# Optimization experiments

Measured on AMD Instinct MI355X. Metric: run time of the kernel, lower is better.

Reference implementation:

```python
import jax, jax.numpy as jnp
import numpy as np

BIG = 1e9  # masks out invalid points in the NN search


def _pixel_grid(H, W, dtype):
    xs, ys = jnp.meshgrid(jnp.arange(W, dtype=dtype), jnp.arange(H, dtype=dtype), indexing='xy')
    return jnp.stack([xs.ravel(), ys.ravel(), jnp.ones(H * W, dtype)], axis=0)  # [3, N]


def _project(depth, K, pose_src, pose_dst, pix):
    """depth [B,1,H,W] -> (points in src cam frame [B,3,N], same points in dst cam frame [B,3,N])."""
    B = depth.shape[0]
    N = pix.shape[1]
    d = depth.reshape(B, 1, N)
    cam = jnp.einsum('bij,jn->bin', jnp.linalg.inv(K), pix) * d          # back-project
    homog = jnp.concatenate([cam, jnp.ones((B, 1, N), cam.dtype)], axis=1)
    T = jnp.einsum('bij,bjk->bik', jnp.linalg.inv(pose_dst), pose_src)   # dst <- src
    dst = jnp.einsum('bij,bjn->bin', T, homog)
    return cam, dst[:, :3]


def _masked_chamfer(a, b, ma, mb):
    """a [N,3], b [M,3], ma [N], mb [M] (0/1 floats). Squared-distance bidirectional chamfer,
    mean over valid points in each direction (pytorch3d chamfer_distance semantics on the
    masked subsets)."""
    d2 = jnp.sum(a * a, -1)[:, None] + jnp.sum(b * b, -1)[None, :] - 2.0 * (a @ b.T)  # [N,M]
    d_ab = jnp.min(d2 + (1.0 - mb)[None, :] * BIG, axis=1)  # NN in b for each a
    d_ba = jnp.min(d2 + (1.0 - ma)[:, None] * BIG, axis=0)  # NN in a for each b
    na = jnp.maximum(jnp.sum(ma), 1.0)
    nb = jnp.maximum(jnp.sum(mb), 1.0)
    return jnp.sum(d_ab * ma) / na + jnp.sum(d_ba * mb) / nb


def setup_inputs() -> dict:
    B, V, H, W = 2, 3, 64, 64
    key = jax.random.key(0)
    k1, k2, k3 = jax.random.split(key, 3)
    views = jax.random.normal(k1, (B, V, 3, H, W), jnp.float32)
    depth_maps = jax.random.uniform(k2, (B, V, 1, H, W), jnp.float32, 1.0, 4.0)
    masks = (jax.random.uniform(k3, (B, V, 1, H, W)) < 0.5).astype(jnp.float32)
    # pinhole intrinsics
    K = np.array([[64.0, 0.0, 32.0], [0.0, 64.0, 32.0], [0.0, 0.0, 1.0]], np.float32)
    intrinsics = jnp.asarray(np.tile(K, (B, 1, 1)))
    # valid SE(3) poses via Rodrigues
    rng = np.random.default_rng(0)
    poses = np.tile(np.eye(4, dtype=np.float32), (B, V, 1, 1))
    for b in range(B):
        for v in range(V):
            ax = rng.normal(size=3); ax = ax / np.linalg.norm(ax)
            ang = rng.uniform(-0.3, 0.3)
            Kx = np.array([[0, -ax[2], ax[1]], [ax[2], 0, -ax[0]], [-ax[1], ax[0], 0]])
            R = np.eye(3) + np.sin(ang) * Kx + (1 - np.cos(ang)) * (Kx @ Kx)
            poses[b, v, :3, :3] = R.astype(np.float32)
            poses[b, v, :3, 3] = rng.uniform(-0.5, 0.5, 3).astype(np.float32)
    return {"views": views, "poses": jnp.asarray(poses), "masks": masks,
            "intrinsics": intrinsics, "depth_maps": depth_maps, "num_views": 3}


def reference(views, poses, masks, intrinsics, depth_maps, num_views):
    B, V, _, H, W = depth_maps.shape
    pix = _pixel_grid(H, W, depth_maps.dtype)
    ref_pose = poses[:, 0]
    ref_mask = masks[:, 0].reshape(B, -1)
    ref_depth = depth_maps[:, 0]
    chamfer = jax.vmap(_masked_chamfer)
    geometric_loss = 0.0
    for i in range(1, num_views):
        tgt_mask = masks[:, i].reshape(B, -1)
        target_coord, proj_t2r = _project(depth_maps[:, i], intrinsics, poses[:, i], ref_pose, pix)
        ref_coord, proj_r2t = _project(ref_depth, intrinsics, ref_pose, poses[:, i], pix)
        fwd = chamfer(ref_coord.transpose(0, 2, 1), proj_t2r.transpose(0, 2, 1), ref_mask, tgt_mask)
        bwd = chamfer(target_coord.transpose(0, 2, 1), proj_r2t.transpose(0, 2, 1), tgt_mask, ref_mask)
        geometric_loss = geometric_loss + jnp.sum(fwd + bwd)
    return geometric_loss / (4.0 * B * (num_views - 1))
```

## Files before the change

### kernel.cpp

```cpp
#include <hip/hip_runtime.h>
#include <math.h>

#define Bb 2
#define Vv 3
#define Nn 4096
#define NDIR 16
#define NRB 32
#define RPB 128
#define NBLKS (NDIR*NRB)
#define PADW 1.5e38f


__device__ __forceinline__ void slots_for_dir(int dir, int* sA, int* sB){
    int k = dir & 3, bi = dir >> 2, b = bi >> 1;
    switch (k){
        case 0:  *sA = b;       *sB = 6 + bi;  break;
        case 1:  *sA = 6 + bi;  *sB = b;       break;
        case 2:  *sA = 2 + bi;  *sB = 10 + bi; break;
        default: *sA = 10 + bi; *sB = 2 + bi;  break;
    }
}

__device__ __forceinline__ void build_matrix(int slot,
                                             const float* __restrict__ poses,
                                             const float* __restrict__ intr,
                                             float* M, float* tv, int* bOut, int* vOut){
    int type, b, im1;
    if (slot < 2)      { type = 0; b = slot;         im1 = 0; }
    else if (slot < 6) { type = 1; b = (slot-2)>>1;  im1 = (slot-2)&1; }
    else if (slot < 10){ type = 2; b = (slot-6)>>1;  im1 = (slot-6)&1; }
    else               { type = 3; b = (slot-10)>>1; im1 = (slot-10)&1; }
    int vi = im1 + 1;
    *bOut = b;
    *vOut = (type==0 || type==3) ? 0 : vi;

    const float* Km = intr + b*9;
    float ka=Km[0],kb=Km[1],kc=Km[2],kd=Km[3],ke=Km[4],kf=Km[5],kg=Km[6],kh=Km[7],ki=Km[8];
    float c00=(ke*ki-kf*kh), c10=-(kd*ki-kf*kg), c20=(kd*kh-ke*kg);
    float det = ka*c00 + kb*c10 + kc*c20, iv = 1.0f/det;
    float Ki[9] = { c00*iv, -(kb*ki-kc*kh)*iv,  (kb*kf-kc*ke)*iv,
                    c10*iv,  (ka*ki-kc*kg)*iv, -(ka*kf-kc*kd)*iv,
                    c20*iv, -(ka*kh-kb*kg)*iv,  (ka*ke-kb*kd)*iv };
    tv[0] = tv[1] = tv[2] = 0.f;
    if (type < 2){
        #pragma unroll
        for (int i = 0; i < 9; ++i) M[i] = Ki[i];
        return;
    }
    const float* P0 = poses + (b*Vv + 0)*16;
    const float* Pi = poses + (b*Vv + vi)*16;
    float R[9];
    if (type == 2){
        #pragma unroll
        for (int r = 0; r < 3; ++r){
            #pragma unroll
            for (int c = 0; c < 3; ++c)
                R[r*3+c] = P0[0*4+r]*Pi[0*4+c] + P0[1*4+r]*Pi[1*4+c] + P0[2*4+r]*Pi[2*4+c];
            tv[r] = P0[0*4+r]*(Pi[3]-P0[3]) + P0[1*4+r]*(Pi[7]-P0[7]) + P0[2*4+r]*(Pi[11]-P0[11]);
        }
    } else {
        #pragma unroll
        for (int r = 0; r < 3; ++r){
            #pragma unroll
            for (int c = 0; c < 3; ++c)
                R[r*3+c] = Pi[0*4+r]*P0[0*4+c] + Pi[1*4+r]*P0[1*4+c] + Pi[2*4+r]*P0[2*4+c];
            tv[r] = Pi[0*4+r]*(P0[3]-Pi[3]) + Pi[1*4+r]*(P0[7]-Pi[7]) + Pi[2*4+r]*(P0[11]-Pi[11]);
        }
    }
    #pragma unroll
    for (int r = 0; r < 3; ++r)
        #pragma unroll
        for (int c = 0; c < 3; ++c)
            M[r*3+c] = R[r*3+0]*Ki[0*3+c] + R[r*3+1]*Ki[1*3+c] + R[r*3+2]*Ki[2*3+c];
}

__global__ void __launch_bounds__(256) fused_kernel(const float* __restrict__ poses,
                                                    const float* __restrict__ masks,
                                                    const float* __restrict__ intr,
                                                    const float* __restrict__ depth,
                                                    float* __restrict__ ws,
                                                    float* __restrict__ out){
    __shared__ float4 sB[Nn + 16];
    __shared__ float4 sA[RPB];
    __shared__ int   wsum[4];
    __shared__ float sred[32];

    int bid = blockIdx.x;
    int rowblk = bid & (NRB-1);
    int dir    = bid >> 5;
    int slotA, slotB;
    slots_for_dir(dir, &slotA, &slotB);

    int tid = threadIdx.x;
    int lane = tid & 63, wv = tid >> 6;

    float MA[9], tA[3], MB[9], tB[3];
    int b, vA, vB, bdummy;
    build_matrix(slotA, poses, intr, MA, tA, &b, &vA);
    build_matrix(slotB, poses, intr, MB, tB, &bdummy, &vB);

    unsigned flA = 0; int tsA = 0;
    {
        const float* mb = masks + (b*Vv + vA)*Nn + tid*16;
        #pragma unroll
        for (int q = 0; q < 4; ++q){
            float4 m4 = *(const float4*)(mb + q*4);
            const float* mv = (const float*)&m4;
            #pragma unroll
            for (int r = 0; r < 4; ++r)
                if (mv[r] > 0.5f){ flA |= 1u << (q*4 + r); ++tsA; }
        }
    }
    int inc = tsA;
    #pragma unroll
    for (int off = 1; off < 64; off <<= 1){
        int t = __shfl_up(inc, off, 64);
        if (lane >= off) inc += t;
    }
    if (lane == 63) wsum[wv] = inc;
    __syncthreads();
    int base = inc - tsA;
    #pragma unroll
    for (int w = 0; w < 4; ++w) if (w < wv) base += wsum[w];
    int cntA = wsum[0] + wsum[1] + wsum[2] + wsum[3];

    int lo = rowblk * RPB;
    int nRows = min(cntA - lo, RPB);
    float partial = 0.f;

    if (nRows > 0){
        {
            const float* dbase = depth + (b*Vv + vA)*Nn;
            int p = base;
            #pragma unroll
            for (int k = 0; k < 16; ++k){
                if (flA & (1u << k)){
                    int rel = p - lo;
                    if (rel >= 0 && rel < RPB){
                        int n = tid*16 + k;
                        float d = dbase[n];
                        float x = (float)(n & 63), y = (float)(n >> 6);
                        float ux = fmaf(MA[0],x, fmaf(MA[1],y, MA[2]));
                        float uy = fmaf(MA[3],x, fmaf(MA[4],y, MA[5]));
                        float uz = fmaf(MA[6],x, fmaf(MA[7],y, MA[8]));
                        float px = fmaf(ux,d,tA[0]), py = fmaf(uy,d,tA[1]), pz = fmaf(uz,d,tA[2]);
                        sA[rel] = make_float4(px,py,pz, 0.5f*(px*px+py*py+pz*pz));
                    }
                    ++p;
                }
            }
        }
        __syncthreads();

        unsigned flB = 0; int tsB = 0;
        float dv[16];
        {
            const float* mb = masks + (b*Vv + vB)*Nn + tid*16;
            const float* db = depth + (b*Vv + vB)*Nn + tid*16;
            #pragma unroll
            for (int q = 0; q < 4; ++q){
                float4 m4 = *(const float4*)(mb + q*4);
                float4 d4 = *(const float4*)(db + q*4);
                const float* mv = (const float*)&m4;
                const float* dd = (const float*)&d4;
                #pragma unroll
                for (int r = 0; r < 4; ++r){
                    dv[q*4+r] = dd[r];
                    if (mv[r] > 0.5f){ flB |= 1u << (q*4 + r); ++tsB; }
                }
            }
        }
        int incB = tsB;
        #pragma unroll
        for (int off = 1; off < 64; off <<= 1){
            int t = __shfl_up(incB, off, 64);
            if (lane >= off) incB += t;
        }
        if (lane == 63) wsum[wv] = incB;
        __syncthreads();
        int baseB = incB - tsB;
        #pragma unroll
        for (int w = 0; w < 4; ++w) if (w < wv) baseB += wsum[w];
        int cntB = wsum[0] + wsum[1] + wsum[2] + wsum[3];

        {
            int p = baseB;
            #pragma unroll
            for (int k = 0; k < 16; ++k){
                if (flB & (1u << k)){
                    int n = tid*16 + k;
                    float d = dv[k];
                    float x = (float)(n & 63), y = (float)(n >> 6);
                    float ux = fmaf(MB[0],x, fmaf(MB[1],y, MB[2]));
                    float uy = fmaf(MB[3],x, fmaf(MB[4],y, MB[5]));
                    float uz = fmaf(MB[6],x, fmaf(MB[7],y, MB[8]));
                    float px = fmaf(ux,d,tB[0]), py = fmaf(uy,d,tB[1]), pz = fmaf(uz,d,tB[2]);
                    sB[p++] = make_float4(px,py,pz, 0.5f*(px*px+py*py+pz*pz));
                }
            }
        }
        int cntBp = (cntB + 15) & ~15;
        if (tid < cntBp - cntB) sB[cntB + tid] = make_float4(0.f, 0.f, 0.f, PADW);
        __syncthreads();

        int rowgrp = tid >> 3, colpart = tid & 7;
        int rbase = rowgrp * 4;
        float4 a0 = sA[rbase+0], a1 = sA[rbase+1], a2 = sA[rbase+2], a3 = sA[rbase+3];
        float m0 = -3.0e38f, m1 = -3.0e38f, m2 = -3.0e38f, m3 = -3.0e38f;

        int nIter = cntBp >> 4;
        const float4* sbp = sB + colpart;
        #pragma unroll 2
        for (int j = 0; j < nIter; ++j){
            float4 c0 = sbp[16*j];
            float4 c1 = sbp[16*j + 8];
            float u00 = fmaf(a0.z,c0.z, fmaf(a0.y,c0.y, fmaf(a0.x,c0.x, -c0.w)));
            float u01 = fmaf(a0.z,c1.z, fmaf(a0.y,c1.y, fmaf(a0.x,c1.x, -c1.w)));
            float u10 = fmaf(a1.z,c0.z, fmaf(a1.y,c0.y, fmaf(a1.x,c0.x, -c0.w)));
            float u11 = fmaf(a1.z,c1.z, fmaf(a1.y,c1.y, fmaf(a1.x,c1.x, -c1.w)));
            float u20 = fmaf(a2.z,c0.z, fmaf(a2.y,c0.y, fmaf(a2.x,c0.x, -c0.w)));
            float u21 = fmaf(a2.z,c1.z, fmaf(a2.y,c1.y, fmaf(a2.x,c1.x, -c1.w)));
            float u30 = fmaf(a3.z,c0.z, fmaf(a3.y,c0.y, fmaf(a3.x,c0.x, -c0.w)));
            float u31 = fmaf(a3.z,c1.z, fmaf(a3.y,c1.y, fmaf(a3.x,c1.x, -c1.w)));
            m0 = fmaxf(fmaxf(u00, u01), m0);
            m1 = fmaxf(fmaxf(u10, u11), m1);
            m2 = fmaxf(fmaxf(u20, u21), m2);
            m3 = fmaxf(fmaxf(u30, u31), m3);
        }
        #pragma unroll
        for (int off = 1; off < 8; off <<= 1){
            m0 = fmaxf(m0, __shfl_xor(m0, off, 64));
            m1 = fmaxf(m1, __shfl_xor(m1, off, 64));
            m2 = fmaxf(m2, __shfl_xor(m2, off, 64));
            m3 = fmaxf(m3, __shfl_xor(m3, off, 64));
        }
        if (colpart == 0){
            float s = 0.f;
            if (rbase + 0 < nRows) s += 2.0f*(a0.w - m0);
            if (rbase + 1 < nRows) s += 2.0f*(a1.w - m1);
            if (rbase + 2 < nRows) s += 2.0f*(a2.w - m2);
            if (rbase + 3 < nRows) s += 2.0f*(a3.w - m3);
            sred[rowgrp] = s;
        }
        __syncthreads();
        if (tid == 0){
            float tsum = 0.f;
            #pragma unroll
            for (int g = 0; g < 16; ++g) tsum += sred[g] + sred[g+16];
            partial = tsum / (fmaxf((float)cntA, 1.0f) * 16.0f);
        }
    }

    unsigned* wsu = (unsigned*)ws;
    if (tid == 0){
        unsigned pb = __float_as_uint(partial);
        atomicExch(&wsu[bid], pb);
        atomicExch(&wsu[NBLKS + bid], ~pb);
    }
    if (bid != 0) return;

    __syncthreads();
    float p0, p1;
    {
        unsigned va, vb;
        for (;;){
            va = atomicAdd(&wsu[tid], 0u);
            vb = atomicAdd(&wsu[NBLKS + tid], 0u);
            if (va == ~vb) break;
            __builtin_amdgcn_s_sleep(1);
        }
        p0 = __uint_as_float(va);
        for (;;){
            va = atomicAdd(&wsu[tid + 256], 0u);
            vb = atomicAdd(&wsu[NBLKS + tid + 256], 0u);
            if (va == ~vb) break;
            __builtin_amdgcn_s_sleep(1);
        }
        p1 = __uint_as_float(va);
    }
    float v = p0 + p1;
    for (int off = 32; off > 0; off >>= 1) v += __shfl_down(v, off, 64);
    if (lane == 0) sred[wv] = v;
    __syncthreads();
    if (tid == 0) out[0] = sred[0] + sred[1] + sred[2] + sred[3];
}

extern "C" void kernel_launch(void* const* d_in, const int* in_sizes, int n_in,
                              void* d_out, int out_size, void* d_ws, size_t ws_size,
                              hipStream_t stream) {
    const float* poses = (const float*)d_in[1];
    const float* masks = (const float*)d_in[2];
    const float* intr  = (const float*)d_in[3];
    const float* depth = (const float*)d_in[4];
    float* ws  = (float*)d_ws;
    float* out = (float*)d_out;

    fused_kernel<<<NBLKS, 256, 0, stream>>>(poses, masks, intr, depth, ws, out);
}
```

Measured before the change: 24.52 us.

## Switch B point cloud to SoA LDS layout with packed FP32 FMA inner loop

Stores the B-side points as four separate shared arrays (x, y, z, negated half-norm) instead of float4, and computes two column dot products per instruction using inline v_pk_fma_f32 asm on float2 loads. It also preloads A-side depth in the same vectorized pass as the mask load, and reorders the block index so that direction varies fastest. The aim is to halve FMA instruction count in the O(N·M) inner loop and make the LDS reads denser. The cost is hand-written asm that the compiler cannot schedule around, the loss of the explicit unroll, and a different column-to-thread assignment.

```diff
diff --git a/kernel.cpp b/kernel.cpp
--- a/kernel.cpp
+++ b/kernel.cpp
@@ -10,6 +10,19 @@
 #define NBLKS (NDIR*NRB)
 #define PADW 1.5e38f
 
+
+__device__ __forceinline__ unsigned dummy(){ return 0; }
+
+__device__ __forceinline__ float2 pk3fma(float2 ax2, float2 ay2, float2 az2,
+                                         float2 xp, float2 yp, float2 zp, float2 wp){
+    float2 u;
+    asm("v_pk_fma_f32 %0, %1, %4, %7\n\t"
+        "v_pk_fma_f32 %0, %2, %5, %0\n\t"
+        "v_pk_fma_f32 %0, %3, %6, %0"
+        : "=&v"(u)
+        : "v"(ax2), "v"(ay2), "v"(az2), "v"(xp), "v"(yp), "v"(zp), "v"(wp));
+    return u;
+}
 
 __device__ __forceinline__ void slots_for_dir(int dir, int* sA, int* sB){
     int k = dir & 3, bi = dir >> 2, b = bi >> 1;
@@ -80,14 +93,17 @@
                                                     const float* __restrict__ depth,
                                                     float* __restrict__ ws,
                                                     float* __restrict__ out){
-    __shared__ float4 sB[Nn + 16];
+    __shared__ __align__(16) float sbx[Nn + 16];
+    __shared__ __align__(16) float sby[Nn + 16];
+    __shared__ __align__(16) float sbz[Nn + 16];
+    __shared__ __align__(16) float sbw[Nn + 16];
     __shared__ float4 sA[RPB];
     __shared__ int   wsum[4];
     __shared__ float sred[32];
 
     int bid = blockIdx.x;
-    int rowblk = bid & (NRB-1);
-    int dir    = bid >> 5;
+    int dir    = bid & (NDIR-1);
+    int rowblk = bid >> 4;
     int slotA, slotB;
     slots_for_dir(dir, &slotA, &slotB);
 
@@ -100,15 +116,21 @@
     build_matrix(slotB, poses, intr, MB, tB, &bdummy, &vB);
 
     unsigned flA = 0; int tsA = 0;
+    float dvA[16];
     {
         const float* mb = masks + (b*Vv + vA)*Nn + tid*16;
+        const float* db = depth + (b*Vv + vA)*Nn + tid*16;
         #pragma unroll
         for (int q = 0; q < 4; ++q){
             float4 m4 = *(const float4*)(mb + q*4);
+            float4 d4 = *(const float4*)(db + q*4);
             const float* mv = (const float*)&m4;
-            #pragma unroll
-            for (int r = 0; r < 4; ++r)
+            const float* dd = (const float*)&d4;
+            #pragma unroll
+            for (int r = 0; r < 4; ++r){
+                dvA[q*4+r] = dd[r];
                 if (mv[r] > 0.5f){ flA |= 1u << (q*4 + r); ++tsA; }
+            }
         }
     }
     int inc = tsA;
@@ -130,7 +152,6 @@
 
     if (nRows > 0){
         {
-            const float* dbase = depth + (b*Vv + vA)*Nn;
             int p = base;
             #pragma unroll
             for (int k = 0; k < 16; ++k){
@@ -138,7 +159,7 @@
                     int rel = p - lo;
                     if (rel >= 0 && rel < RPB){
                         int n = tid*16 + k;
-                        float d = dbase[n];
+                        float d = dvA[k];
                         float x = (float)(n & 63), y = (float)(n >> 6);
                         float ux = fmaf(MA[0],x, fmaf(MA[1],y, MA[2]));
                         float uy = fmaf(MA[3],x, fmaf(MA[4],y, MA[5]));
@@ -195,37 +216,41 @@
                     float uy = fmaf(MB[3],x, fmaf(MB[4],y, MB[5]));
                     float uz = fmaf(MB[6],x, fmaf(MB[7],y, MB[8]));
                     float px = fmaf(ux,d,tB[0]), py = fmaf(uy,d,tB[1]), pz = fmaf(uz,d,tB[2]);
-                    sB[p++] = make_float4(px,py,pz, 0.5f*(px*px+py*py+pz*pz));
+                    sbx[p] = px; sby[p] = py; sbz[p] = pz;
+                    sbw[p] = -0.5f*(px*px + py*py + pz*pz);
+                    ++p;
                 }
             }
         }
         int cntBp = (cntB + 15) & ~15;
-        if (tid < cntBp - cntB) sB[cntB + tid] = make_float4(0.f, 0.f, 0.f, PADW);
+        if (tid < cntBp - cntB){
+            sbx[cntB+tid] = 0.f; sby[cntB+tid] = 0.f; sbz[cntB+tid] = 0.f;
+            sbw[cntB+tid] = -PADW;
+        }
         __syncthreads();
 
         int rowgrp = tid >> 3, colpart = tid & 7;
         int rbase = rowgrp * 4;
         float4 a0 = sA[rbase+0], a1 = sA[rbase+1], a2 = sA[rbase+2], a3 = sA[rbase+3];
+        float2 a0x = {a0.x,a0.x}, a0y = {a0.y,a0.y}, a0z = {a0.z,a0.z};
+        float2 a1x = {a1.x,a1.x}, a1y = {a1.y,a1.y}, a1z = {a1.z,a1.z};
+        float2 a2x = {a2.x,a2.x}, a2y = {a2.y,a2.y}, a2z = {a2.z,a2.z};
+        float2 a3x = {a3.x,a3.x}, a3y = {a3.y,a3.y}, a3z = {a3.z,a3.z};
         float m0 = -3.0e38f, m1 = -3.0e38f, m2 = -3.0e38f, m3 = -3.0e38f;
 
         int nIter = cntBp >> 4;
-        const float4* sbp = sB + colpart;
-        #pragma unroll 2
+        int o = 2*colpart;
         for (int j = 0; j < nIter; ++j){
-            float4 c0 = sbp[16*j];
-            float4 c1 = sbp[16*j + 8];
-            float u00 = fmaf(a0.z,c0.z, fmaf(a0.y,c0.y, fmaf(a0.x,c0.x, -c0.w)));
-            float u01 = fmaf(a0.z,c1.z, fmaf(a0.y,c1.y, fmaf(a0.x,c1.x, -c1.w)));
-            float u10 = fmaf(a1.z,c0.z, fmaf(a1.y,c0.y, fmaf(a1.x,c0.x, -c0.w)));
-            float u11 = fmaf(a1.z,c1.z, fmaf(a1.y,c1.y, fmaf(a1.x,c1.x, -c1.w)));
-            float u20 = fmaf(a2.z,c0.z, fmaf(a2.y,c0.y, fmaf(a2.x,c0.x, -c0.w)));
-            float u21 = fmaf(a2.z,c1.z, fmaf(a2.y,c1.y, fmaf(a2.x,c1.x, -c1.w)));
-            float u30 = fmaf(a3.z,c0.z, fmaf(a3.y,c0.y, fmaf(a3.x,c0.x, -c0.w)));
-            float u31 = fmaf(a3.z,c1.z, fmaf(a3.y,c1.y, fmaf(a3.x,c1.x, -c1.w)));
-            m0 = fmaxf(fmaxf(u00, u01), m0);
-            m1 = fmaxf(fmaxf(u10, u11), m1);
-            m2 = fmaxf(fmaxf(u20, u21), m2);
-            m3 = fmaxf(fmaxf(u30, u31), m3);
+            float2 xp = *(const float2*)&sbx[o];
+            float2 yp = *(const float2*)&sby[o];
+            float2 zp = *(const float2*)&sbz[o];
+            float2 wp = *(const float2*)&sbw[o];
+            float2 u;
+            u = pk3fma(a0x,a0y,a0z, xp,yp,zp, wp); m0 = fmaxf(fmaxf(u.x,u.y), m0);
+            u = pk3fma(a1x,a1y,a1z, xp,yp,zp, wp); m1 = fmaxf(fmaxf(u.x,u.y), m1);
+            u = pk3fma(a2x,a2y,a2z, xp,yp,zp, wp); m2 = fmaxf(fmaxf(u.x,u.y), m2);
+            u = pk3fma(a3x,a3y,a3z, xp,yp,zp, wp); m3 = fmaxf(fmaxf(u.x,u.y), m3);
+            o += 16;
         }
         #pragma unroll
         for (int off = 1; off < 8; off <<= 1){
```

Result: slower. 26.20 us (+6.8%).

## Halve block count, reuse projected B cloud across two row blocks per block

Applied to the files above, without the earlier changes.

Blocks drop from 512 to 256. Each block now builds the projected B point cloud in shared memory once and loops over up to two row blocks of A, so the B projection and prefix scan are no longer recomputed per row block. The inner tile grows from 4 rows by 8 column lanes to 8 rows by 16 column lanes, which raises register reuse of the A points. Direction now comes from the low bits of the block index, so neighbouring blocks work on different directions. The cost is less parallelism, more registers per thread, and serial work inside blocks that get both row blocks.

```diff
diff --git a/kernel.cpp b/kernel.cpp
--- a/kernel.cpp
+++ b/kernel.cpp
@@ -5,7 +5,7 @@
 #define Vv 3
 #define Nn 4096
 #define NDIR 16
-#define NRB 32
+#define NRB 16
 #define RPB 128
 #define NBLKS (NDIR*NRB)
 #define PADW 1.5e38f
@@ -80,14 +80,15 @@
                                                     const float* __restrict__ depth,
                                                     float* __restrict__ ws,
                                                     float* __restrict__ out){
-    __shared__ float4 sB[Nn + 16];
+    __shared__ float4 sB[Nn + 32];
     __shared__ float4 sA[RPB];
     __shared__ int   wsum[4];
-    __shared__ float sred[32];
+    __shared__ float sred[16];
+    __shared__ float fred[4];
 
     int bid = blockIdx.x;
-    int rowblk = bid & (NRB-1);
-    int dir    = bid >> 5;
+    int dir    = bid & (NDIR-1);
+    int rowblk = bid >> 4;
     int slotA, slotB;
     slots_for_dir(dir, &slotA, &slotB);
 
@@ -100,15 +101,21 @@
     build_matrix(slotB, poses, intr, MB, tB, &bdummy, &vB);
 
     unsigned flA = 0; int tsA = 0;
+    float dvA[16];
     {
         const float* mb = masks + (b*Vv + vA)*Nn + tid*16;
+        const float* db = depth + (b*Vv + vA)*Nn + tid*16;
         #pragma unroll
         for (int q = 0; q < 4; ++q){
             float4 m4 = *(const float4*)(mb + q*4);
+            float4 d4 = *(const float4*)(db + q*4);
             const float* mv = (const float*)&m4;
-            #pragma unroll
-            for (int r = 0; r < 4; ++r)
+            const float* dd = (const float*)&d4;
+            #pragma unroll
+            for (int r = 0; r < 4; ++r){
+                dvA[q*4+r] = dd[r];
                 if (mv[r] > 0.5f){ flA |= 1u << (q*4 + r); ++tsA; }
+            }
         }
     }
     int inc = tsA;
@@ -123,14 +130,67 @@
     #pragma unroll
     for (int w = 0; w < 4; ++w) if (w < wv) base += wsum[w];
     int cntA = wsum[0] + wsum[1] + wsum[2] + wsum[3];
-
-    int lo = rowblk * RPB;
-    int nRows = min(cntA - lo, RPB);
-    float partial = 0.f;
-
-    if (nRows > 0){
+    __syncthreads();
+
+    unsigned flB = 0; int tsB = 0;
+    float dv[16];
+    {
+        const float* mb = masks + (b*Vv + vB)*Nn + tid*16;
+        const float* db = depth + (b*Vv + vB)*Nn + tid*16;
+        #pragma unroll
+        for (int q = 0; q < 4; ++q){
+            float4 m4 = *(const float4*)(mb + q*4);
+            float4 d4 = *(const float4*)(db + q*4);
+            const float* mv = (const float*)&m4;
+            const float* dd = (const float*)&d4;
+            #pragma unroll
+            for (int r = 0; r < 4; ++r){
+                dv[q*4+r] = dd[r];
+                if (mv[r] > 0.5f){ flB |= 1u << (q*4 + r); ++tsB; }
+            }
+        }
+    }
+    int incB = tsB;
+    #pragma unroll
+    for (int off = 1; off < 64; off <<= 1){
+        int t = __shfl_up(incB, off, 64);
+        if (lane >= off) incB += t;
+    }
+    if (lane == 63) wsum[wv] = incB;
+    __syncthreads();
+    int baseB = incB - tsB;
+    #pragma unroll
+    for (int w = 0; w < 4; ++w) if (w < wv) baseB += wsum[w];
+    int cntB = wsum[0] + wsum[1] + wsum[2] + wsum[3];
+
+    {
+        int p = baseB;
+        #pragma unroll
+        for (int k = 0; k < 16; ++k){
+            if (flB & (1u << k)){
+                int n = tid*16 + k;
+                float d = dv[k];
+                float x = (float)(n & 63), y = (float)(n >> 6);
+                float ux = fmaf(MB[0],x, fmaf(MB[1],y, MB[2]));
+                float uy = fmaf(MB[3],x, fmaf(MB[4],y, MB[5]));
+                float uz = fmaf(MB[6],x, fmaf(MB[7],y, MB[8]));
+                float px = fmaf(ux,d,tB[0]), py = fmaf(uy,d,tB[1]), pz = fmaf(uz,d,tB[2]);
+                sB[p++] = make_float4(px, py, pz, 0.5f*(px*px + py*py + pz*pz));
+            }
+        }
+    }
+    int cntBp = (cntB + 31) & ~31;
+    for (int t = cntB + tid; t < cntBp; t += 256)
+        sB[t] = make_float4(0.f, 0.f, 0.f, PADW);
+
+    float tsum = 0.f;
+
+    for (int s = rowblk; s < 32; s += 16){
+        int lo = s * RPB;
+        int nRows = min(cntA - lo, RPB);
+        if (nRows <= 0) break;
+
         {
-            const float* dbase = depth + (b*Vv + vA)*Nn;
             int p = base;
             #pragma unroll
             for (int k = 0; k < 16; ++k){
@@ -138,7 +198,7 @@
                     int rel = p - lo;
                     if (rel >= 0 && rel < RPB){
                         int n = tid*16 + k;
-                        float d = dbase[n];
+                        float d = dvA[k];
                         float x = (float)(n & 63), y = (float)(n >> 6);
                         float ux = fmaf(MA[0],x, fmaf(MA[1],y, MA[2]));
                         float uy = fmaf(MA[3],x, fmaf(MA[4],y, MA[5]));
@@ -152,107 +212,51 @@
         }
         __syncthreads();
 
-        unsigned flB = 0; int tsB = 0;
-        float dv[16];
-        {
-            const float* mb = masks + (b*Vv + vB)*Nn + tid*16;
-            const float* db = depth + (b*Vv + vB)*Nn + tid*16;
-            #pragma unroll
-            for (int q = 0; q < 4; ++q){
-                float4 m4 = *(const float4*)(mb + q*4);
-                float4 d4 = *(const float4*)(db + q*4);
-                const float* mv = (const float*)&m4;
-                const float* dd = (const float*)&d4;
-                #pragma unroll
-                for (int r = 0; r < 4; ++r){
-                    dv[q*4+r] = dd[r];
-                    if (mv[r] > 0.5f){ flB |= 1u << (q*4 + r); ++tsB; }
-                }
-            }
-        }
-        int incB = tsB;
-        #pragma unroll
-        for (int off = 1; off < 64; off <<= 1){
-            int t = __shfl_up(incB, off, 64);
-            if (lane >= off) incB += t;
-        }
-        if (lane == 63) wsum[wv] = incB;
-        __syncthreads();
-        int baseB = incB - tsB;
-        #pragma unroll
-        for (int w = 0; w < 4; ++w) if (w < wv) baseB += wsum[w];
-        int cntB = wsum[0] + wsum[1] + wsum[2] + wsum[3];
-
-        {
-            int p = baseB;
-            #pragma unroll
-            for (int k = 0; k < 16; ++k){
-                if (flB & (1u << k)){
-                    int n = tid*16 + k;
-                    float d = dv[k];
-                    float x = (float)(n & 63), y = (float)(n >> 6);
-                    float ux = fmaf(MB[0],x, fmaf(MB[1],y, MB[2]));
-                    float uy = fmaf(MB[3],x, fmaf(MB[4],y, MB[5]));
-                    float uz = fmaf(MB[6],x, fmaf(MB[7],y, MB[8]));
-                    float px = fmaf(ux,d,tB[0]), py = fmaf(uy,d,tB[1]), pz = fmaf(uz,d,tB[2]);
-                    sB[p++] = make_float4(px,py,pz, 0.5f*(px*px+py*py+pz*pz));
-                }
-            }
-        }
-        int cntBp = (cntB + 15) & ~15;
-        if (tid < cntBp - cntB) sB[cntB + tid] = make_float4(0.f, 0.f, 0.f, PADW);
-        __syncthreads();
-
-        int rowgrp = tid >> 3, colpart = tid & 7;
-        int rbase = rowgrp * 4;
-        float4 a0 = sA[rbase+0], a1 = sA[rbase+1], a2 = sA[rbase+2], a3 = sA[rbase+3];
-        float m0 = -3.0e38f, m1 = -3.0e38f, m2 = -3.0e38f, m3 = -3.0e38f;
-
-        int nIter = cntBp >> 4;
-        const float4* sbp = sB + colpart;
-        #pragma unroll 2
+        int rowgrp = tid >> 4, colpart = tid & 15;
+        int rbase = rowgrp * 8;
+        float4 a[8];
+        #pragma unroll
+        for (int r = 0; r < 8; ++r) a[r] = sA[rbase + r];
+        float m[8];
+        #pragma unroll
+        for (int r = 0; r < 8; ++r) m[r] = -3.0e38f;
+
+        int nIter = cntBp >> 5;
+        const float4* sb0 = sB + colpart;
         for (int j = 0; j < nIter; ++j){
-            float4 c0 = sbp[16*j];
-            float4 c1 = sbp[16*j + 8];
-            float u00 = fmaf(a0.z,c0.z, fmaf(a0.y,c0.y, fmaf(a0.x,c0.x, -c0.w)));
-            float u01 = fmaf(a0.z,c1.z, fmaf(a0.y,c1.y, fmaf(a0.x,c1.x, -c1.w)));
-            float u10 = fmaf(a1.z,c0.z, fmaf(a1.y,c0.y, fmaf(a1.x,c0.x, -c0.w)));
-            float u11 = fmaf(a1.z,c1.z, fmaf(a1.y,c1.y, fmaf(a1.x,c1.x, -c1.w)));
-            float u20 = fmaf(a2.z,c0.z, fmaf(a2.y,c0.y, fmaf(a2.x,c0.x, -c0.w)));
-            float u21 = fmaf(a2.z,c1.z, fmaf(a2.y,c1.y, fmaf(a2.x,c1.x, -c1.w)));
-            float u30 = fmaf(a3.z,c0.z, fmaf(a3.y,c0.y, fmaf(a3.x,c0.x, -c0.w)));
-            float u31 = fmaf(a3.z,c1.z, fmaf(a3.y,c1.y, fmaf(a3.x,c1.x, -c1.w)));
-            m0 = fmaxf(fmaxf(u00, u01), m0);
-            m1 = fmaxf(fmaxf(u10, u11), m1);
-            m2 = fmaxf(fmaxf(u20, u21), m2);
-            m3 = fmaxf(fmaxf(u30, u31), m3);
-        }
-        #pragma unroll
-        for (int off = 1; off < 8; off <<= 1){
-            m0 = fmaxf(m0, __shfl_xor(m0, off, 64));
-            m1 = fmaxf(m1, __shfl_xor(m1, off, 64));
-            m2 = fmaxf(m2, __shfl_xor(m2, off, 64));
-            m3 = fmaxf(m3, __shfl_xor(m3, off, 64));
+            float4 c0 = sb0[32*j];
+            float4 c1 = sb0[32*j + 16];
+            #pragma unroll
+            for (int r = 0; r < 8; ++r){
+                float u0 = fmaf(a[r].z,c0.z, fmaf(a[r].y,c0.y, fmaf(a[r].x,c0.x, -c0.w)));
+                float u1 = fmaf(a[r].z,c1.z, fmaf(a[r].y,c1.y, fmaf(a[r].x,c1.x, -c1.w)));
+                m[r] = fmaxf(fmaxf(u0, u1), m[r]);
+            }
+        }
+        #pragma unroll
+        for (int off = 1; off < 16; off <<= 1){
+            #pragma unroll
+            for (int r = 0; r < 8; ++r)
+                m[r] = fmaxf(m[r], __shfl_xor(m[r], off, 64));
         }
         if (colpart == 0){
-            float s = 0.f;
-            if (rbase + 0 < nRows) s += 2.0f*(a0.w - m0);
-            if (rbase + 1 < nRows) s += 2.0f*(a1.w - m1);
-            if (rbase + 2 < nRows) s += 2.0f*(a2.w - m2);
-            if (rbase + 3 < nRows) s += 2.0f*(a3.w - m3);
-            sred[rowgrp] = s;
+            float sl = 0.f;
+            #pragma unroll
+            for (int r = 0; r < 8; ++r)
+                if (rbase + r < nRows) sl += 2.0f*(a[r].w - m[r]);
+            sred[rowgrp] = sl;
         }
         __syncthreads();
         if (tid == 0){
-            float tsum = 0.f;
-            #pragma unroll
-            for (int g = 0; g < 16; ++g) tsum += sred[g] + sred[g+16];
-            partial = tsum / (fmaxf((float)cntA, 1.0f) * 16.0f);
-        }
+            #pragma unroll
+            for (int g = 0; g < 16; ++g) tsum += sred[g];
+        }
+        __syncthreads();
     }
 
     unsigned* wsu = (unsigned*)ws;
     if (tid == 0){
+        float partial = tsum / (fmaxf((float)cntA, 1.0f) * 16.0f);
         unsigned pb = __float_as_uint(partial);
         atomicExch(&wsu[bid], pb);
         atomicExch(&wsu[NBLKS + bid], ~pb);
@@ -260,29 +264,18 @@
     if (bid != 0) return;
 
     __syncthreads();
-    float p0, p1;
-    {
-        unsigned va, vb;
-        for (;;){
-            va = atomicAdd(&wsu[tid], 0u);
-            vb = atomicAdd(&wsu[NBLKS + tid], 0u);
-            if (va == ~vb) break;
-            __builtin_amdgcn_s_sleep(1);
-        }
-        p0 = __uint_as_float(va);
-        for (;;){
-            va = atomicAdd(&wsu[tid + 256], 0u);
-            vb = atomicAdd(&wsu[NBLKS + tid + 256], 0u);
-            if (va == ~vb) break;
-            __builtin_amdgcn_s_sleep(1);
-        }
-        p1 = __uint_as_float(va);
-    }
-    float v = p0 + p1;
+    unsigned va, vb;
+    for (;;){
+        va = atomicAdd(&wsu[tid], 0u);
+        vb = atomicAdd(&wsu[NBLKS + tid], 0u);
+        if (va == ~vb) break;
+        __builtin_amdgcn_s_sleep(1);
+    }
+    float v = __uint_as_float(va);
     for (int off = 32; off > 0; off >>= 1) v += __shfl_down(v, off, 64);
-    if (lane == 0) sred[wv] = v;
-    __syncthreads();
-    if (tid == 0) out[0] = sred[0] + sred[1] + sred[2] + sred[3];
+    if (lane == 0) fred[wv] = v;
+    __syncthreads();
+    if (tid == 0) out[0] = fred[0] + fred[1] + fred[2] + fred[3];
 }
 
 extern "C" void kernel_launch(void* const* d_in, const int* in_sizes, int n_in,
```

Result: slower. 30.42 us (+24.0%).
